# Kernel tuning notes

Hardware: AMD Instinct MI355X
Metric: run time of the kernel (lower is better)

Reference implementation:

```python
import jax, jax.numpy as jnp
import numpy as np

N_ANCHORS = 250000
IMG_H, IMG_W = 1024, 1024
PRE_NMS = 6000    # num_pre_nms_test (inference path, training=False)
POST_NMS = 300    # num_post_nms_test
IOU_THR = 0.7


def setup_inputs() -> dict:
    key = jax.random.key(0)
    k1, k2, k3, k4, k5 = jax.random.split(key, 5)
    bboxes_txtytwth = jax.random.normal(k1, (N_ANCHORS, 4), dtype=jnp.float32) * 0.1
    # anchors as (ymin, xmin, ymax, xmax) scattered over the image
    cy = jax.random.uniform(k2, (N_ANCHORS,), dtype=jnp.float32) * IMG_H
    cx = jax.random.uniform(k3, (N_ANCHORS,), dtype=jnp.float32) * IMG_W
    ah = 32.0 + jax.random.uniform(k4, (N_ANCHORS,), dtype=jnp.float32) * 224.0
    aw = 32.0 + jax.random.uniform(k5, (N_ANCHORS,), dtype=jnp.float32) * 224.0
    anchors = jnp.stack([cy - 0.5 * ah, cx - 0.5 * aw,
                         cy + 0.5 * ah, cx + 0.5 * aw], axis=1)
    scores = jax.random.normal(jax.random.fold_in(key, 7), (N_ANCHORS,), dtype=jnp.float32)
    return {
        "bboxes_txtytwth": bboxes_txtytwth,
        "anchors": anchors,
        "scores": scores,
        "image_height": IMG_H,
        "image_width": IMG_W,
        "extractor_stride": 16,
    }


def _decode_bbox(anchors, deltas):
    # anchors: [N,4] (ymin,xmin,ymax,xmax); deltas: [N,4] (ty,tx,th,tw)
    h = anchors[:, 2] - anchors[:, 0]
    w = anchors[:, 3] - anchors[:, 1]
    cy = anchors[:, 0] + 0.5 * h
    cx = anchors[:, 1] + 0.5 * w
    ty, tx, th, tw = deltas[:, 0], deltas[:, 1], deltas[:, 2], deltas[:, 3]
    ncy = ty * h + cy
    ncx = tx * w + cx
    nh = jnp.exp(th) * h
    nw = jnp.exp(tw) * w
    return jnp.stack([ncy - 0.5 * nh, ncx - 0.5 * nw,
                      ncy + 0.5 * nh, ncx + 0.5 * nw], axis=1)


def _iou_matrix(b):
    # b: [K,4] -> [K,K] pairwise IoU
    area = (b[:, 2] - b[:, 0]) * (b[:, 3] - b[:, 1])
    iy = jnp.maximum(0.0, jnp.minimum(b[:, None, 2], b[None, :, 2]) -
                     jnp.maximum(b[:, None, 0], b[None, :, 0]))
    ix = jnp.maximum(0.0, jnp.minimum(b[:, None, 3], b[None, :, 3]) -
                     jnp.maximum(b[:, None, 1], b[None, :, 1]))
    inter = iy * ix
    return inter / (area[:, None] + area[None, :] - inter + 1e-9)


def _rpn_proposal(bboxes_txtytwth, anchors, scores, image_height, image_width,
                  extractor_stride):
    # 1) decode
    boxes = _decode_bbox(anchors, bboxes_txtytwth)
    # 2) clip to image + min-edge filter (filter implemented as score mask)
    ymin = jnp.clip(boxes[:, 0], 0.0, image_height)
    xmin = jnp.clip(boxes[:, 1], 0.0, image_width)
    ymax = jnp.clip(boxes[:, 2], 0.0, image_height)
    xmax = jnp.clip(boxes[:, 3], 0.0, image_width)
    boxes = jnp.stack([ymin, xmin, ymax, xmax], axis=1)
    valid = ((ymax - ymin) >= extractor_stride) & ((xmax - xmin) >= extractor_stride)
    masked_scores = jnp.where(valid, scores, -jnp.inf)
    # 3) pre-NMS top-k (sorted descending by score)
    top_scores, top_idx = jax.lax.top_k(masked_scores, PRE_NMS)
    top_boxes = boxes[top_idx]                      # [PRE_NMS,4]
    valid_k = jnp.isfinite(top_scores)
    # 4) greedy NMS over score-sorted boxes
    iou = _iou_matrix(top_boxes)                    # [PRE_NMS, PRE_NMS]
    order = jnp.arange(PRE_NMS)

    def body(i, suppressed):
        alive_i = jnp.logical_not(suppressed[i]) & valid_k[i]
        return suppressed | (alive_i & (iou[i] > IOU_THR) & (order > i))

    suppressed = jax.lax.fori_loop(0, PRE_NMS, body,
                                   jnp.zeros((PRE_NMS,), dtype=bool))
    keep = jnp.logical_not(suppressed) & valid_k
    # 5) first POST_NMS kept boxes (already score-ordered), fixed-shape output
    rank = jnp.cumsum(keep) - 1                     # position among kept
    tgt = jnp.where(keep & (rank < POST_NMS), rank, POST_NMS)
    out = jnp.zeros((POST_NMS + 1, 4), dtype=top_boxes.dtype).at[tgt].set(top_boxes)
    return out[:POST_NMS]                           # [POST_NMS,4], zero-padded


def reference(bboxes_txtytwth, anchors, scores, image_height, image_width,
              extractor_stride):
    return _rpn_proposal(bboxes_txtytwth, anchors, scores,
                         float(image_height), float(image_width),
                         float(extractor_stride))
```

## Files before the change

kernel.cpp:

```cpp
#include <hip/hip_runtime.h>

#pragma clang fp contract(off)

#define N_PRE   6000
#define N_POST  300
#define NW      94
#define SELCAP  7936
#define RS_BLK  124
#define NBIN    16384
#define DSHIFT  18
#define HPART   64

struct SelState {
    unsigned int thr;
};

__global__ void decode_kernel(const float4* __restrict__ deltas,
                              const float4* __restrict__ anchors,
                              const float*  __restrict__ scores,
                              const int* __restrict__ ph, const int* __restrict__ pw,
                              const int* __restrict__ ps,
                              unsigned int* __restrict__ s32out,
                              float4* __restrict__ boxes,
                              unsigned long long* __restrict__ sel,
                              unsigned long long* __restrict__ valid_words,
                              unsigned int* __restrict__ counter, int N)
{
#pragma clang fp contract(off)
    if (blockIdx.x == 0) {
        for (int t = threadIdx.x; t < SELCAP; t += 256) sel[t] = 0ull;
    } else if (blockIdx.x == 1) {
        if (threadIdx.x < 128) valid_words[threadIdx.x] = 0ull;
        if (threadIdx.x == 0) *counter = 0u;
    }
    int i = blockIdx.x * blockDim.x + threadIdx.x;
    if (i >= N) return;
    float H = (float)(*ph), W = (float)(*pw), S = (float)(*ps);
    float4 d = deltas[i];
    float4 a = anchors[i];
    float h = a.z - a.x, w = a.w - a.y;
    float cy = a.x + 0.5f * h, cx = a.y + 0.5f * w;
    float ncy = d.x * h + cy;
    float ncx = d.y * w + cx;
    float eh = (float)exp((double)d.z);
    float ew = (float)exp((double)d.w);
    float nh = eh * h;
    float nw = ew * w;
    float ymin = ncy - 0.5f * nh, xmin = ncx - 0.5f * nw;
    float ymax = ncy + 0.5f * nh, xmax = ncx + 0.5f * nw;
    ymin = fminf(fmaxf(ymin, 0.0f), H);
    xmin = fminf(fmaxf(xmin, 0.0f), W);
    ymax = fminf(fmaxf(ymax, 0.0f), H);
    xmax = fminf(fmaxf(xmax, 0.0f), W);
    bool valid = (ymax - ymin >= S) && (xmax - xmin >= S);
    float sc = scores[i];
    unsigned int bits = __float_as_uint(sc);
    unsigned int s32;
    if (!valid) s32 = 0x007FFFFFu;
    else        s32 = (bits & 0x80000000u) ? ~bits : (bits | 0x80000000u);
    s32out[i] = s32;
    boxes[i]  = make_float4(ymin, xmin, ymax, xmax);
}

__global__ __launch_bounds__(256) void hist_part(const unsigned int* __restrict__ s32in,
                                                 unsigned int* __restrict__ phist, int N)
{
    __shared__ unsigned int lh[NBIN];
    int tid = threadIdx.x;
    for (int j = tid; j < NBIN; j += 256) lh[j] = 0u;
    __syncthreads();
    for (int i = blockIdx.x * 256 + tid; i < N; i += HPART * 256)
        atomicAdd(&lh[s32in[i] >> DSHIFT], 1u);
    __syncthreads();
    unsigned int* dst = phist + blockIdx.x * NBIN;
    for (int j = tid; j < NBIN; j += 256) dst[j] = lh[j];
}

__global__ __launch_bounds__(256) void hist_reduce(const unsigned int* __restrict__ phist,
                                                   unsigned int* __restrict__ hist)
{
    int j = blockIdx.x * 256 + threadIdx.x;
    unsigned int s = 0;
#pragma unroll 8
    for (int b = 0; b < HPART; b++) s += phist[b * NBIN + j];
    hist[j] = s;
}

__global__ __launch_bounds__(1024) void pick_pass(const unsigned int* __restrict__ hist,
                                                  SelState* __restrict__ state)
{
    __shared__ unsigned int wsum[16];
    __shared__ int sel_chunk;
    __shared__ unsigned int sel_above;
    int tid = threadIdx.x, lane = tid & 63, wave = tid >> 6;
    const unsigned int k = 6000u;

    unsigned int s = 0;
    int base = tid * 16;
#pragma unroll
    for (int i = 0; i < 16; i++) s += hist[base + i];
    unsigned int S = s;
    for (int d = 1; d < 64; d <<= 1) {
        unsigned int t = __shfl_down(S, d);
        if (lane + d < 64) S += t;
    }
    if (lane == 0) wsum[wave] = S;
    __syncthreads();
    unsigned int above = 0;
    for (int w2 = wave + 1; w2 < 16; w2++) above += wsum[w2];
    unsigned int F  = S + above;
    unsigned int Fn = F - s;
    if (Fn < k && k <= F) { sel_chunk = tid; sel_above = Fn; }
    __syncthreads();
    int c = sel_chunk;
    unsigned int acc = sel_above;
    if (wave == 0 && lane < 16) {
        unsigned int b = hist[c * 16 + lane];
        unsigned int B = b;
        for (int d = 1; d < 16; d <<= 1) {
            unsigned int t = __shfl_down(B, d);
            if (lane + d < 16) B += t;
        }
        unsigned int Bn = B - b;
        unsigned int kk = k - acc;
        if (Bn < kk && kk <= B) state->thr = (unsigned int)(c * 16 + lane);
    }
}

__global__ void compact_kernel(const unsigned int* __restrict__ s32in,
                               const SelState* __restrict__ state,
                               unsigned long long* __restrict__ sel,
                               unsigned int* __restrict__ counter, int N)
{
    int i = blockIdx.x * blockDim.x + threadIdx.x;
    if (i >= N) return;
    unsigned int s32 = s32in[i];
    if ((s32 >> DSHIFT) >= state->thr) {
        unsigned int p = atomicAdd(counter, 1u);
        if (p < SELCAP)
            sel[p] = ((unsigned long long)s32 << 32) |
                     (unsigned long long)(~(unsigned int)i);
    }
}

__global__ __launch_bounds__(256) void rank_scatter(
    const unsigned long long* __restrict__ sel,
    const float4* __restrict__ boxes,
    float4* __restrict__ boxes_sorted,
    unsigned long long* __restrict__ valid_words, int N)
{
    __shared__ __align__(16) unsigned long long kbuf[SELCAP];
    __shared__ unsigned int cnt4[4][64];
    int tid = threadIdx.x;
    for (int t = tid; t < SELCAP; t += 256) kbuf[t] = sel[t];
    __syncthreads();
    int lane = tid & 63;
    int slice = tid >> 6;
    int i = blockIdx.x * 64 + lane;
    unsigned long long my = kbuf[i];
    const int SL = SELCAP / 4;
    int j0 = slice * SL;
    unsigned int c = 0;
#pragma unroll 8
    for (int j = j0; j < j0 + SL; j += 2) {
        ulonglong2 kk = *reinterpret_cast<const ulonglong2*>(&kbuf[j]);
        c += (kk.x > my) || (kk.x == my && j < i);
        c += (kk.y > my) || (kk.y == my && (j + 1) < i);
    }
    cnt4[slice][lane] = c;
    __syncthreads();
    if (tid < 64) {
        unsigned int rank = cnt4[0][tid] + cnt4[1][tid] + cnt4[2][tid] + cnt4[3][tid];
        unsigned long long key = kbuf[blockIdx.x * 64 + tid];
        if (key != 0ull && rank < N_PRE) {
            unsigned int s32 = (unsigned int)(key >> 32);
            unsigned int ii  = ~(unsigned int)(key & 0xFFFFFFFFull);
            float4 b = (ii < (unsigned int)N) ? boxes[ii] : make_float4(0.f,0.f,0.f,0.f);
            boxes_sorted[rank] = b;
            bool v = (s32 != 0x007FFFFFu) && (ii < (unsigned int)N);
            if (v) atomicOr(&valid_words[rank >> 6], 1ull << (rank & 63));
        }
    }
}

__global__ __launch_bounds__(64) void mask_kernel(const float4* __restrict__ boxes_sorted,
                                                  unsigned long long* __restrict__ mask)
{
#pragma clang fp contract(off)
    int rb = blockIdx.y, cb = blockIdx.x;
    if (cb < rb) return;
    __shared__ float4 cbox[64];
    int tid = threadIdx.x;
    int col0 = cb * 64;
    int c = col0 + tid;
    cbox[tid] = (c < N_PRE) ? boxes_sorted[c] : make_float4(0.f, 0.f, 0.f, 0.f);
    __syncthreads();
    int i = rb * 64 + tid;
    if (i >= N_PRE) return;
    float4 bi = boxes_sorted[i];
    float area_i = (bi.z - bi.x) * (bi.w - bi.y);
    unsigned long long word = 0ull;
#pragma unroll 8
    for (int j = 0; j < 64; j++) {
        float4 bj = cbox[j];
        float iy = fminf(bi.z, bj.z) - fmaxf(bi.x, bj.x);
        iy = fmaxf(iy, 0.0f);
        float ix = fminf(bi.w, bj.w) - fmaxf(bi.y, bj.y);
        ix = fmaxf(ix, 0.0f);
        float inter = iy * ix;
        float area_j = (bj.z - bj.x) * (bj.w - bj.y);
        float iou = inter / (((area_i + area_j) - inter) + 1e-9f);
        if ((col0 + j) > i && iou > 0.7f) word |= (1ull << j);
    }
    mask[(size_t)i * NW + cb] = word;
}

__global__ __launch_bounds__(64) void nms_seq(const unsigned long long* __restrict__ mask,
                                              const unsigned long long* __restrict__ valid_words,
                                              const float4* __restrict__ boxes_sorted,
                                              float* __restrict__ out)
{
#pragma clang fp contract(off)
    int lane = threadIdx.x;
    float4* out4 = reinterpret_cast<float4*>(out);

    for (int t = lane; t < N_POST; t += 64)
        out4[t] = make_float4(0.f, 0.f, 0.f, 0.f);

    unsigned long long vw0 = valid_words[lane];
    unsigned long long vw1 = (lane < NW - 64) ? valid_words[64 + lane] : 0ull;
    unsigned long long rem0 = ~vw0;
    unsigned long long rem1 = ~vw1;

    unsigned long long pA_lo[8] = {0,0,0,0,0,0,0,0}, pA_hi[8] = {0,0,0,0,0,0,0,0};
    unsigned long long pB_lo[8] = {0,0,0,0,0,0,0,0}, pB_hi[8] = {0,0,0,0,0,0,0,0};

    unsigned long long carry = 0ull;
    int rank = 0;

    int row0 = lane;
    unsigned long long dg_d = mask[(size_t)row0 * NW + 0];
    unsigned long long dg_b = mask[(size_t)row0 * NW + 1];
    float4 cb = boxes_sorted[lane];

#define WORD_STEP(WV, PLO, PHI)                                                 \
    {                                                                           \
        int w = (WV);                                                           \
               \
        rem0 |= ((PLO[0]|PLO[1])|(PLO[2]|PLO[3]))|((PLO[4]|PLO[5])|(PLO[6]|PLO[7])); \
        rem1 |= ((PHI[0]|PHI[1])|(PHI[2]|PHI[3]))|((PHI[4]|PHI[5])|(PHI[6]|PHI[7])); \
             \
        unsigned long long dgn_d = 0ull, dgn_b = 0ull;                          \
        float4 cbn = cb;                                                        \
        if (w + 1 < NW) {                                                       \
            int rown = (w + 1) * 64 + lane;                                     \
            if (rown > N_PRE - 1) rown = N_PRE - 1;                             \
            dgn_d = mask[(size_t)rown * NW + (w + 1)];                          \
            dgn_b = mask[(size_t)rown * NW + (w + 2)];                          \
            cbn = boxes_sorted[(w + 1) * 64 + lane];                            \
        }                                                                       \
        unsigned long long remw = (w < 64) ? __shfl(rem0, w) : __shfl(rem1, w - 64); \
        unsigned long long vw   = (w < 64) ? __shfl(vw0, w)  : __shfl(vw1, w - 64); \
        unsigned long long alive = vw & ~remw & ~carry;                         \
        carry = 0ull;                                                           \
        unsigned long long keptb = 0ull;                                        \
        while (alive) {                                                         \
            int b = __builtin_ctzll(alive);                   \
            unsigned long long dxb = __shfl(dg_d, b);                           \
            unsigned long long dyb = __shfl(dg_b, b);                           \
            if (lane == b) out4[rank] = cb;                                     \
            keptb |= 1ull << b;                                                 \
            rank++;                                                             \
            if (rank >= N_POST) break;                                          \
            alive &= ~(dxb | (1ull << b));                                      \
            carry |= dyb;                                                       \
        }                                                                       \
        if (rank >= N_POST) break;                                              \
                     \
        {                                                                       \
            int kc = __popcll(keptb);                                           \
            unsigned long long kb = keptb;                                      \
            _Pragma("unroll")                                                   \
            for (int sslot = 0; sslot < 8; sslot++) {                           \
                if (sslot < kc) {                                               \
                    int bb = __builtin_ctzll(kb); kb &= kb - 1ull;              \
                    const unsigned long long* rp = mask + (size_t)(w * 64 + bb) * NW; \
                    PLO[sslot] = rp[lane];                                      \
                    PHI[sslot] = (lane < NW - 64) ? rp[64 + lane] : 0ull;       \
                } else { PLO[sslot] = 0ull; PHI[sslot] = 0ull; }                \
            }                                                                   \
            while (kb) {            \
                int bb = __builtin_ctzll(kb); kb &= kb - 1ull;                  \
                const unsigned long long* rp = mask + (size_t)(w * 64 + bb) * NW; \
                rem0 |= rp[lane];                                               \
                if (lane < NW - 64) rem1 |= rp[64 + lane];                      \
            }                                                                   \
        }                                                                       \
        dg_d = dgn_d; dg_b = dgn_b; cb = cbn;                                   \
    }

    for (int w2 = 0; w2 < NW; w2 += 2) {
        WORD_STEP(w2,     pA_lo, pA_hi)
        WORD_STEP(w2 + 1, pB_lo, pB_hi)
    }
#undef WORD_STEP
}

extern "C" void kernel_launch(void* const* d_in, const int* in_sizes, int n_in,
                              void* d_out, int out_size, void* d_ws, size_t ws_size,
                              hipStream_t stream)
{
    const float4* deltas  = (const float4*)d_in[0];
    const float4* anchors = (const float4*)d_in[1];
    const float*  scores  = (const float*)d_in[2];
    const int* ph = (const int*)d_in[3];
    const int* pw = (const int*)d_in[4];
    const int* ps = (const int*)d_in[5];
    int N = in_sizes[2];

    char* base = (char*)d_ws;
    size_t off = 0;
    auto alloc = [&](size_t sz) -> void* {
        void* p = base + off;
        off = (off + sz + 255) & ~(size_t)255;
        return p;
    };
    unsigned int* s32buf = (unsigned int*)alloc(sizeof(unsigned int) * (size_t)N);
    float4* boxes = (float4*)alloc(sizeof(float4) * (size_t)N);
    unsigned int* phist = (unsigned int*)alloc((size_t)HPART * NBIN * sizeof(unsigned int));
    unsigned int* hist = (unsigned int*)alloc(NBIN * sizeof(unsigned int));
    SelState* state = (SelState*)alloc(256);
    unsigned int* counter = (unsigned int*)alloc(256);
    unsigned long long* valid_words = (unsigned long long*)alloc(128 * 8);
    unsigned long long* sel = (unsigned long long*)alloc(sizeof(unsigned long long) * SELCAP);
    float4* boxes_sorted = (float4*)alloc(sizeof(float4) * 6016);
    unsigned long long* mask = (unsigned long long*)alloc(sizeof(unsigned long long) * ((size_t)N_PRE * NW + 32));

    int nb = (N + 255) / 256;
    decode_kernel<<<nb, 256, 0, stream>>>(deltas, anchors, scores, ph, pw, ps,
                                          s32buf, boxes, sel, valid_words, counter, N);
    hist_part<<<HPART, 256, 0, stream>>>(s32buf, phist, N);
    hist_reduce<<<NBIN / 256, 256, 0, stream>>>(phist, hist);
    pick_pass<<<1, 1024, 0, stream>>>(hist, state);
    compact_kernel<<<nb, 256, 0, stream>>>(s32buf, state, sel, counter, N);
    rank_scatter<<<RS_BLK, 256, 0, stream>>>(sel, boxes, boxes_sorted, valid_words, N);
    mask_kernel<<<dim3(NW, NW), 64, 0, stream>>>(boxes_sorted, mask);
    nms_seq<<<1, 64, 0, stream>>>(mask, valid_words, boxes_sorted, (float*)d_out);
}
```

Baseline: 313.3 us.

## Transpose diagonal mask blocks for ballot-based NMS and widen rank_scatter blocks

The mask kernel now also writes transposed copies of the diagonal and next-band 64x64 bit blocks, built with wave ballots. The serial NMS loop reads these so each lane tests its own suppression bit, and a single ballot replaces the two 64-bit shuffles per kept box on the dependent chain. Scalar readlanes replace shuffles for the broadcast of the removed and valid words. rank_scatter runs 1024 threads per block with 16 slices per key, summed through LDS atomics, to raise parallelism in the ranking count; this adds atomic contention and the extra transpose work in the mask kernel.

```diff
diff --git a/kernel.cpp b/kernel.cpp
--- a/kernel.cpp
+++ b/kernel.cpp
@@ -14,6 +14,12 @@
 struct SelState {
     unsigned int thr;
 };
+
+static __device__ __forceinline__ unsigned long long readlane64(unsigned long long v, int l) {
+    unsigned lo = __builtin_amdgcn_readlane((unsigned)v, l);
+    unsigned hi = __builtin_amdgcn_readlane((unsigned)(v >> 32), l);
+    return ((unsigned long long)hi << 32) | lo;
+}
 
 __global__ void decode_kernel(const float4* __restrict__ deltas,
                               const float4* __restrict__ anchors,
@@ -143,22 +149,23 @@
     }
 }
 
-__global__ __launch_bounds__(256) void rank_scatter(
+__global__ __launch_bounds__(1024) void rank_scatter(
     const unsigned long long* __restrict__ sel,
     const float4* __restrict__ boxes,
     float4* __restrict__ boxes_sorted,
     unsigned long long* __restrict__ valid_words, int N)
 {
     __shared__ __align__(16) unsigned long long kbuf[SELCAP];
-    __shared__ unsigned int cnt4[4][64];
+    __shared__ unsigned int cnt[64];
     int tid = threadIdx.x;
-    for (int t = tid; t < SELCAP; t += 256) kbuf[t] = sel[t];
+    if (tid < 64) cnt[tid] = 0u;
+    for (int t = tid; t < SELCAP; t += 1024) kbuf[t] = sel[t];
     __syncthreads();
     int lane = tid & 63;
     int slice = tid >> 6;
     int i = blockIdx.x * 64 + lane;
     unsigned long long my = kbuf[i];
-    const int SL = SELCAP / 4;
+    const int SL = SELCAP / 16;
     int j0 = slice * SL;
     unsigned int c = 0;
 #pragma unroll 8
@@ -167,10 +174,10 @@
         c += (kk.x > my) || (kk.x == my && j < i);
         c += (kk.y > my) || (kk.y == my && (j + 1) < i);
     }
-    cnt4[slice][lane] = c;
+    atomicAdd(&cnt[lane], c);
     __syncthreads();
     if (tid < 64) {
-        unsigned int rank = cnt4[0][tid] + cnt4[1][tid] + cnt4[2][tid] + cnt4[3][tid];
+        unsigned int rank = cnt[tid];
         unsigned long long key = kbuf[blockIdx.x * 64 + tid];
         if (key != 0ull && rank < N_PRE) {
             unsigned int s32 = (unsigned int)(key >> 32);
@@ -184,7 +191,9 @@
 }
 
 __global__ __launch_bounds__(64) void mask_kernel(const float4* __restrict__ boxes_sorted,
-                                                  unsigned long long* __restrict__ mask)
+                                                  unsigned long long* __restrict__ mask,
+                                                  unsigned long long* __restrict__ diagT,
+                                                  unsigned long long* __restrict__ bandT)
 {
 #pragma clang fp contract(off)
     int rb = blockIdx.y, cb = blockIdx.x;
@@ -213,9 +222,21 @@
         if ((col0 + j) > i && iou > 0.7f) word |= (1ull << j);
     }
     mask[(size_t)i * NW + cb] = word;
+
+    if (cb == rb || cb == rb + 1) {
+        unsigned long long colw = 0ull;
+        for (int jj = 0; jj < 64; jj++) {
+            unsigned long long t = __ballot((unsigned int)((word >> jj) & 1ull));
+            if (tid == jj) colw = t;
+        }
+        if (cb == rb) diagT[rb * 64 + tid] = colw;
+        else          bandT[rb * 64 + tid] = colw;
+    }
 }
 
 __global__ __launch_bounds__(64) void nms_seq(const unsigned long long* __restrict__ mask,
+                                              const unsigned long long* __restrict__ diagT,
+                                              const unsigned long long* __restrict__ bandT,
                                               const unsigned long long* __restrict__ valid_words,
                                               const float4* __restrict__ boxes_sorted,
                                               float* __restrict__ out)
@@ -235,12 +256,11 @@
     unsigned long long pA_lo[8] = {0,0,0,0,0,0,0,0}, pA_hi[8] = {0,0,0,0,0,0,0,0};
     unsigned long long pB_lo[8] = {0,0,0,0,0,0,0,0}, pB_hi[8] = {0,0,0,0,0,0,0,0};
 
-    unsigned long long carry = 0ull;
+    unsigned long long carryword = 0ull;
     int rank = 0;
 
-    int row0 = lane;
-    unsigned long long dg_d = mask[(size_t)row0 * NW + 0];
-    unsigned long long dg_b = mask[(size_t)row0 * NW + 1];
+    unsigned long long dT = diagT[lane];
+    unsigned long long bT = bandT[lane];
     float4 cb = boxes_sorted[lane];
 
 #define WORD_STEP(WV, PLO, PHI)                                                 \
@@ -249,33 +269,34 @@
                \
         rem0 |= ((PLO[0]|PLO[1])|(PLO[2]|PLO[3]))|((PLO[4]|PLO[5])|(PLO[6]|PLO[7])); \
         rem1 |= ((PHI[0]|PHI[1])|(PHI[2]|PHI[3]))|((PHI[4]|PHI[5])|(PHI[6]|PHI[7])); \
-             \
-        unsigned long long dgn_d = 0ull, dgn_b = 0ull;                          \
+               \
+        unsigned long long dTn = 0ull, bTn = 0ull;                              \
         float4 cbn = cb;                                                        \
         if (w + 1 < NW) {                                                       \
-            int rown = (w + 1) * 64 + lane;                                     \
-            if (rown > N_PRE - 1) rown = N_PRE - 1;                             \
-            dgn_d = mask[(size_t)rown * NW + (w + 1)];                          \
-            dgn_b = mask[(size_t)rown * NW + (w + 2)];                          \
+            dTn = diagT[(w + 1) * 64 + lane];                                   \
+            bTn = bandT[(w + 1) * 64 + lane];                                   \
             cbn = boxes_sorted[(w + 1) * 64 + lane];                            \
         }                                                                       \
-        unsigned long long remw = (w < 64) ? __shfl(rem0, w) : __shfl(rem1, w - 64); \
-        unsigned long long vw   = (w < 64) ? __shfl(vw0, w)  : __shfl(vw1, w - 64); \
-        unsigned long long alive = vw & ~remw & ~carry;                         \
-        carry = 0ull;                                                           \
+        unsigned long long remw = (w < 64) ? readlane64(rem0, w)                \
+                                           : readlane64(rem1, w - 64);          \
+        unsigned long long vw   = (w < 64) ? readlane64(vw0, w)                 \
+                                           : readlane64(vw1, w - 64);           \
+        unsigned long long alive = vw & ~remw & ~carryword;                     \
+        unsigned int carryacc = 0u;                                             \
         unsigned long long keptb = 0ull;                                        \
         while (alive) {                                                         \
             int b = __builtin_ctzll(alive);                   \
-            unsigned long long dxb = __shfl(dg_d, b);                           \
-            unsigned long long dyb = __shfl(dg_b, b);                           \
+            unsigned int supme = (unsigned int)((dT >> b) & 1ull);              \
+            carryacc |= (unsigned int)((bT >> b) & 1ull);                       \
             if (lane == b) out4[rank] = cb;                                     \
             keptb |= 1ull << b;                                                 \
             rank++;                                                             \
             if (rank >= N_POST) break;                                          \
-            alive &= ~(dxb | (1ull << b));                                      \
-            carry |= dyb;                                                       \
+            unsigned long long supw = __ballot(supme);                          \
+            alive &= ~(supw | (1ull << b));                                     \
         }                                                                       \
         if (rank >= N_POST) break;                                              \
+        carryword = __ballot(carryacc);                                         \
                      \
         {                                                                       \
             int kc = __popcll(keptb);                                           \
@@ -296,7 +317,7 @@
                 if (lane < NW - 64) rem1 |= rp[64 + lane];                      \
             }                                                                   \
         }                                                                       \
-        dg_d = dgn_d; dg_b = dgn_b; cb = cbn;                                   \
+        dT = dTn; bT = bTn; cb = cbn;                                           \
     }
 
     for (int w2 = 0; w2 < NW; w2 += 2) {
@@ -334,6 +355,8 @@
     unsigned long long* valid_words = (unsigned long long*)alloc(128 * 8);
     unsigned long long* sel = (unsigned long long*)alloc(sizeof(unsigned long long) * SELCAP);
     float4* boxes_sorted = (float4*)alloc(sizeof(float4) * 6016);
+    unsigned long long* diagT = (unsigned long long*)alloc(sizeof(unsigned long long) * NW * 64);
+    unsigned long long* bandT = (unsigned long long*)alloc(sizeof(unsigned long long) * NW * 64);
     unsigned long long* mask = (unsigned long long*)alloc(sizeof(unsigned long long) * ((size_t)N_PRE * NW + 32));
 
     int nb = (N + 255) / 256;
@@ -343,7 +366,7 @@
     hist_reduce<<<NBIN / 256, 256, 0, stream>>>(phist, hist);
     pick_pass<<<1, 1024, 0, stream>>>(hist, state);
     compact_kernel<<<nb, 256, 0, stream>>>(s32buf, state, sel, counter, N);
-    rank_scatter<<<RS_BLK, 256, 0, stream>>>(sel, boxes, boxes_sorted, valid_words, N);
-    mask_kernel<<<dim3(NW, NW), 64, 0, stream>>>(boxes_sorted, mask);
-    nms_seq<<<1, 64, 0, stream>>>(mask, valid_words, boxes_sorted, (float*)d_out);
-}
+    rank_scatter<<<RS_BLK, 1024, 0, stream>>>(sel, boxes, boxes_sorted, valid_words, N);
+    mask_kernel<<<dim3(NW, NW), 64, 0, stream>>>(boxes_sorted, mask, diagT, bandT);
+    nms_seq<<<1, 64, 0, stream>>>(mask, diagT, bandT, valid_words, boxes_sorted, (float*)d_out);
+}
```

Result: faster. 263.4 us (-15.9%).
